# Performance work log

Measured on AMD Instinct MI355X. Metric: run time of the kernel, lower is better.

Reference implementation:

```python
import jax, jax.numpy as jnp
import numpy as np

DIM = 768
NUM_HEADS = 12
HEAD_DIM = DIM // NUM_HEADS
H, W = 16, 64
HK, WK = 7, 11
N = H * W
B = 8
SCALE = HEAD_DIM ** -0.5


def build_local_mask():
    # Vectorized version of the original nested loop: for each token (h,w),
    # positions inside the hk x wk window are visible (0), others -inf.
    h_idx = np.repeat(np.arange(H), W)  # [N]
    w_idx = np.tile(np.arange(W), H)    # [N]
    hh = np.arange(H + HK - 1)
    ww = np.arange(W + WK - 1)
    in_h = (hh[None, :] >= h_idx[:, None]) & (hh[None, :] < h_idx[:, None] + HK)  # [N, H+hk-1]
    in_w = (ww[None, :] >= w_idx[:, None]) & (ww[None, :] < w_idx[:, None] + WK)  # [N, W+wk-1]
    visible = in_h[:, :, None] & in_w[:, None, :]  # [N, H+hk-1, W+wk-1]
    mask_big = np.where(visible, 0.0, 1.0).astype(np.float32)
    mask_crop = mask_big[:, HK // 2:H + HK // 2, WK // 2:W + WK // 2].reshape(N, N)
    mask = np.where(mask_crop < 1.0, mask_crop, np.float32(-np.inf))  # [N, N]
    return jnp.asarray(mask)[None, None]  # [1, 1, N, N]


def setup_inputs() -> dict:
    key = jax.random.key(0)
    k1, k2, k3 = jax.random.split(key, 3)
    x = jax.random.normal(k1, (B, N, DIM), dtype=jnp.float32)
    w_qkv = jax.random.normal(k2, (3 * DIM, DIM), dtype=jnp.float32) * 0.02  # torch Linear weight [out,in]
    w_proj = jax.random.normal(k3, (DIM, DIM), dtype=jnp.float32) * 0.02
    b_proj = jnp.zeros((DIM,), dtype=jnp.float32)
    mask = build_local_mask()
    return {"x": x, "w_qkv": w_qkv, "w_proj": w_proj, "b_proj": b_proj, "mask": mask}


def reference(x, w_qkv, w_proj, b_proj, mask):
    Bx, Nx, C = x.shape
    qkv = jnp.einsum('bnc,oc->bno', x, w_qkv)  # [B, N, 3*dim]
    qkv = qkv.reshape(Bx, Nx, 3, NUM_HEADS, HEAD_DIM).transpose(2, 0, 3, 1, 4)  # [3,B,h,N,d]
    q, k, v = qkv[0] * SCALE, qkv[1], qkv[2]
    attn = jnp.einsum('bhnd,bhmd->bhnm', q, k) + mask  # [B,h,N,N] with local -inf mask
    attn = jax.nn.softmax(attn, axis=-1)
    out = jnp.einsum('bhnm,bhmd->bhnd', attn, v)  # [B,h,N,d]
    out = out.transpose(0, 2, 1, 3).reshape(Bx, Nx, C)
    out = jnp.einsum('bnc,oc->bno', out, w_proj) + b_proj
    return out
```

## Files before the change

### kernel.cpp

```cpp
#include <hip/hip_runtime.h>
#include <hip/hip_bf16.h>
#include <stdint.h>

typedef __bf16 bf16;
typedef __bf16 bf16x8 __attribute__((ext_vector_type(8)));
typedef __bf16 bf16x4 __attribute__((ext_vector_type(4)));
typedef float f32x4 __attribute__((ext_vector_type(4)));

#define KDIM 768
#define NHEAD 12
#define HDIM 64
#define NTOK 1024
#define BATCH 8

#define SWZ(row, b) ((b) ^ (((row) & 7) << 4))

__device__ __forceinline__ void gl_lds16(const bf16* g, bf16* l) {
    __builtin_amdgcn_global_load_lds((const __attribute__((address_space(1))) void*)g,
                                     (__attribute__((address_space(3))) void*)l, 16, 0, 0);
}

__global__ void k_cvt_all(const float* __restrict__ x, const float* __restrict__ wq,
                          const float* __restrict__ wp, bf16* __restrict__ xb,
                          bf16* __restrict__ wqb, bf16* __restrict__ wpb) {
    int b = blockIdx.x;
    const float* src;
    bf16* dst;
    int base;
    if (b < 6144)       { src = x;  dst = xb;  base = b; }
    else if (b < 7872)  { src = wq; dst = wqb; base = b - 6144; }
    else                { src = wp; dst = wpb; base = b - 7872; }
    int i = (base * 256 + threadIdx.x) * 4;
    float4 v = *(const float4*)(src + i);
    bf16x4 o;
    o[0] = (bf16)v.x; o[1] = (bf16)v.y; o[2] = (bf16)v.z; o[3] = (bf16)v.w;
    *(bf16x4*)(dst + i) = o;
}

#define BM 128
#define BN 128
#define BK 32

#define STAGE_G(Ab, Wb, Abuf, Bbuf, k0) do {                                  \
    gl_lds16((Ab) + (size_t)srow * KDIM + (k0) + scol,        (Abuf) + wv * 512);        \
    gl_lds16((Ab) + (size_t)(srow + 64) * KDIM + (k0) + scol, (Abuf) + 2048 + wv * 512); \
    gl_lds16((Wb) + (size_t)srow * KDIM + (k0) + scol,        (Bbuf) + wv * 512);        \
    gl_lds16((Wb) + (size_t)(srow + 64) * KDIM + (k0) + scol, (Bbuf) + 2048 + wv * 512); \
} while (0)

__global__ __launch_bounds__(256) void k_gemm_qkv(
    const bf16* __restrict__ A, const bf16* __restrict__ W,
    bf16* __restrict__ qb, bf16* __restrict__ kb, bf16* __restrict__ vb)
{
    __shared__ bf16 As[2][BM * BK];
    __shared__ bf16 Bs[2][BN * BK];
    const int t = threadIdx.x;
    const int lane = t & 63;
    const int wv = t >> 6;
    const int wr = wv >> 1, wc = wv & 1;
    const int lr = lane & 15, lkb = (lane >> 4) * 8;
    const int bm = blockIdx.x, bn = blockIdx.y;

    const bf16* Ab = A + (size_t)bm * BM * KDIM;
    const bf16* Wb = W + (size_t)bn * BN * KDIM;

    const int srow = t >> 2;
    const int scol = (t & 3) * 8;

    f32x4 acc[4][4] = {};

    STAGE_G(Ab, Wb, As[0], Bs[0], 0);
    __syncthreads();

    int cur = 0;
    for (int k0 = 0; k0 < KDIM; k0 += BK) {
        if (k0 + BK < KDIM)
            STAGE_G(Ab, Wb, As[cur ^ 1], Bs[cur ^ 1], k0 + BK);
        bf16x8 af[4], bfr[4];
#pragma unroll
        for (int m = 0; m < 4; ++m)
            af[m] = *(const bf16x8*)&As[cur][(wr * 64 + m * 16 + lr) * BK + lkb];
#pragma unroll
        for (int n = 0; n < 4; ++n)
            bfr[n] = *(const bf16x8*)&Bs[cur][(wc * 64 + n * 16 + lr) * BK + lkb];
#pragma unroll
        for (int m = 0; m < 4; ++m)
#pragma unroll
            for (int n = 0; n < 4; ++n)
                acc[m][n] = __builtin_amdgcn_mfma_f32_16x16x32_bf16(af[m], bfr[n], acc[m][n], 0, 0, 0);
        __syncthreads();
        cur ^= 1;
    }

    const float QSC = 0.18033688011112042f;
#pragma unroll
    for (int n = 0; n < 4; ++n) {
        int o = bn * BN + wc * 64 + n * 16 + lr;
        int s = o / 768;
        int rem = o - s * 768;
        int head = rem >> 6;
        int d = o & 63;
        bf16* dst = (s == 0) ? qb : ((s == 1) ? kb : vb);
        float sc = (s == 0) ? QSC : 1.0f;
#pragma unroll
        for (int m = 0; m < 4; ++m) {
            int grow = bm * BM + wr * 64 + m * 16 + (lane >> 4) * 4;
            int bidx = grow >> 10;
            int tok = grow & 1023;
            size_t base = (((size_t)bidx * NHEAD + head) * NTOK + tok) * HDIM + d;
#pragma unroll
            for (int r = 0; r < 4; ++r)
                dst[base + (size_t)r * HDIM] = (bf16)(acc[m][n][r] * sc);
        }
    }
}

__global__ __launch_bounds__(256) void k_gemm_proj(
    const bf16* __restrict__ A, const bf16* __restrict__ W,
    const float* __restrict__ bias, float* __restrict__ out)
{
    __shared__ bf16 As[2][BM * BK];
    __shared__ bf16 Bs[2][BN * BK];
    const int t = threadIdx.x;
    const int lane = t & 63;
    const int wv = t >> 6;
    const int wr = wv >> 1, wc = wv & 1;
    const int lr = lane & 15, lkb = (lane >> 4) * 8;
    const int bm = blockIdx.x, bn = blockIdx.y;

    const bf16* Ab = A + (size_t)bm * BM * KDIM;
    const bf16* Wb = W + (size_t)bn * BN * KDIM;

    const int srow = t >> 2;
    const int scol = (t & 3) * 8;

    f32x4 acc[4][4] = {};

    STAGE_G(Ab, Wb, As[0], Bs[0], 0);
    __syncthreads();

    int cur = 0;
    for (int k0 = 0; k0 < KDIM; k0 += BK) {
        if (k0 + BK < KDIM)
            STAGE_G(Ab, Wb, As[cur ^ 1], Bs[cur ^ 1], k0 + BK);
        bf16x8 af[4], bfr[4];
#pragma unroll
        for (int m = 0; m < 4; ++m)
            af[m] = *(const bf16x8*)&As[cur][(wr * 64 + m * 16 + lr) * BK + lkb];
#pragma unroll
        for (int n = 0; n < 4; ++n)
            bfr[n] = *(const bf16x8*)&Bs[cur][(wc * 64 + n * 16 + lr) * BK + lkb];
#pragma unroll
        for (int m = 0; m < 4; ++m)
#pragma unroll
            for (int n = 0; n < 4; ++n)
                acc[m][n] = __builtin_amdgcn_mfma_f32_16x16x32_bf16(af[m], bfr[n], acc[m][n], 0, 0, 0);
        __syncthreads();
        cur ^= 1;
    }

#pragma unroll
    for (int n = 0; n < 4; ++n) {
        int col = bn * BN + wc * 64 + n * 16 + lr;
        float bv = bias[col];
#pragma unroll
        for (int m = 0; m < 4; ++m) {
            int grow = bm * BM + wr * 64 + m * 16 + (lane >> 4) * 4;
#pragma unroll
            for (int r = 0; r < 4; ++r)
                out[(size_t)(grow + r) * KDIM + col] = acc[m][n][r] + bv;
        }
    }
}

__global__ __launch_bounds__(256) void k_attn(
    const bf16* __restrict__ qbuf, const bf16* __restrict__ kbuf,
    const bf16* __restrict__ vbuf, bf16* __restrict__ ob)
{
    const int x = blockIdx.x;
    const int sub = x >> 3;
    const int bh = (x & 7) * 12 + (sub >> 4);
    const int qblk = sub & 15;
    const int head = bh % NHEAD, bidx = bh / NHEAD;
    const bf16* Q  = qbuf + (size_t)bh * NTOK * HDIM;
    const bf16* Kp = kbuf + (size_t)bh * NTOK * HDIM;
    const bf16* Vp = vbuf + (size_t)bh * NTOK * HDIM;

    const int t = threadIdx.x, lane = t & 63, wv = t >> 6;
    const int lr = lane & 15, lg = lane >> 4, lkb = lg * 8;

    __shared__ bf16 Ks[2][64 * 64];
    __shared__ bf16 vT[2][64 * 64];
    __shared__ bf16 pls[4][16 * 64];

    {
        bf16x8 z = {};
        *(bf16x8*)&pls[wv][lane * 16] = z;
        *(bf16x8*)&pls[wv][lane * 16 + 8] = z;
    }

    bf16x8 qf[2];
#pragma unroll
    for (int ks = 0; ks < 2; ++ks)
        qf[ks] = *(const bf16x8*)(Q + (size_t)(qblk * 64 + wv * 16 + lr) * HDIM + ks * 32 + lkb);

    f32x4 acc[4] = {};
    float mrow[4] = {-1e30f, -1e30f, -1e30f, -1e30f};
    float lrow[4] = {0.f, 0.f, 0.f, 0.f};

    const int kh0 = (qblk - 3 < 0) ? 0 : qblk - 3;
    const int kh1 = (qblk + 3 > 15) ? 15 : qblk + 3;

    const int sj = t >> 2;
    const int sd = (t & 3) * 16;

    const bf16* ks0 = Kp + (size_t)(kh0 * 64 + sj) * HDIM + sd;
    const bf16* vs0 = Vp + (size_t)(kh0 * 64 + sj) * HDIM + sd;
    bf16x8 gk0 = *(const bf16x8*)ks0, gk1 = *(const bf16x8*)(ks0 + 8);
    bf16x8 gv0 = *(const bf16x8*)vs0, gv1 = *(const bf16x8*)(vs0 + 8);

    char* pb8 = (char*)pls[wv];
    const int wq0 = wv * 16 + lg * 4;
    int cur = 0;

    for (int kh = kh0; kh <= kh1; ++kh) {
        char* kb8 = (char*)Ks[cur];
        char* vb8 = (char*)vT[cur];
        {
            int kbo = sj * 128 + sd * 2;
            *(bf16x8*)(kb8 + SWZ(sj, kbo)) = gk0;
            *(bf16x8*)(kb8 + SWZ(sj, kbo + 16)) = gk1;
        }
#pragma unroll
        for (int ii = 0; ii < 8; ++ii) {
            int d = sd + ii;
            *(bf16*)(vb8 + SWZ(d, (d << 7) + (sj << 1))) = gv0[ii];
        }
#pragma unroll
        for (int ii = 0; ii < 8; ++ii) {
            int d = sd + 8 + ii;
            *(bf16*)(vb8 + SWZ(d, (d << 7) + (sj << 1))) = gv1[ii];
        }
        if (kh < kh1) {
            const bf16* kn = Kp + (size_t)((kh + 1) * 64 + sj) * HDIM + sd;
            const bf16* vn = Vp + (size_t)((kh + 1) * 64 + sj) * HDIM + sd;
            gk0 = *(const bf16x8*)kn; gk1 = *(const bf16x8*)(kn + 8);
            gv0 = *(const bf16x8*)vn; gv1 = *(const bf16x8*)(vn + 8);
        }
        asm volatile("s_waitcnt lgkmcnt(0)" ::: "memory");
        __builtin_amdgcn_s_barrier();

        f32x4 s[3];
#pragma unroll
        for (int jj = 0; jj < 3; ++jj) {
            int j = wv - 1 + jj;
            if (j >= 0 && j <= 3) {
                int key = j * 16 + lr;
                int kbase = key * 128;
                bf16x8 kf0 = *(const bf16x8*)(kb8 + SWZ(key, kbase + lg * 16));
                bf16x8 kf1 = *(const bf16x8*)(kb8 + SWZ(key, kbase + 64 + lg * 16));
                f32x4 sv = {};
                sv = __builtin_amdgcn_mfma_f32_16x16x32_bf16(qf[0], kf0, sv, 0, 0, 0);
                sv = __builtin_amdgcn_mfma_f32_16x16x32_bf16(qf[1], kf1, sv, 0, 0, 0);
#pragma unroll
                for (int r = 0; r < 4; ++r) {
                    int dw = wq0 + r - key;
                    sv[r] = (dw >= -5 && dw <= 5) ? sv[r] : -1e30f;
                }
                s[jj] = sv;
            } else {
                s[jj] = f32x4{-1e30f, -1e30f, -1e30f, -1e30f};
            }
        }

        float pm[4], scl[4];
#pragma unroll
        for (int r = 0; r < 4; ++r) pm[r] = fmaxf(fmaxf(s[0][r], s[1][r]), s[2][r]);
#pragma unroll
        for (int off = 1; off < 16; off <<= 1)
#pragma unroll
            for (int r = 0; r < 4; ++r) pm[r] = fmaxf(pm[r], __shfl_xor(pm[r], off));
#pragma unroll
        for (int r = 0; r < 4; ++r) {
            float mn = fmaxf(mrow[r], pm[r]);
            scl[r] = exp2f(mrow[r] - mn);
            mrow[r] = mn;
        }
#pragma unroll
        for (int dt = 0; dt < 4; ++dt)
#pragma unroll
            for (int r = 0; r < 4; ++r) acc[dt][r] *= scl[r];

        float psum[4] = {0.f, 0.f, 0.f, 0.f};
#pragma unroll
        for (int jj = 0; jj < 3; ++jj) {
            int j = wv - 1 + jj;
            if (j >= 0 && j <= 3) {
#pragma unroll
                for (int r = 0; r < 4; ++r) {
                    float p = exp2f(s[jj][r] - mrow[r]);
                    psum[r] += p;
                    int row = lg * 4 + r;
                    *(bf16*)(pb8 + SWZ(row, row * 128 + (j * 16 + lr) * 2)) = (bf16)p;
                }
            }
        }
#pragma unroll
        for (int r = 0; r < 4; ++r) lrow[r] = lrow[r] * scl[r] + psum[r];

        bf16x8 pf0 = *(const bf16x8*)(pb8 + SWZ(lr, lr * 128 + lg * 16));
        bf16x8 pf1 = *(const bf16x8*)(pb8 + SWZ(lr, lr * 128 + 64 + lg * 16));
#pragma unroll
        for (int dt = 0; dt < 4; ++dt) {
            int vrow = dt * 16 + lr;
            bf16x8 vf0 = *(const bf16x8*)(vb8 + SWZ(vrow, vrow * 128 + lg * 16));
            bf16x8 vf1 = *(const bf16x8*)(vb8 + SWZ(vrow, vrow * 128 + 64 + lg * 16));
            acc[dt] = __builtin_amdgcn_mfma_f32_16x16x32_bf16(pf0, vf0, acc[dt], 0, 0, 0);
            acc[dt] = __builtin_amdgcn_mfma_f32_16x16x32_bf16(pf1, vf1, acc[dt], 0, 0, 0);
        }
        cur ^= 1;
    }

#pragma unroll
    for (int off = 1; off < 16; off <<= 1)
#pragma unroll
        for (int r = 0; r < 4; ++r) lrow[r] += __shfl_xor(lrow[r], off);

#pragma unroll
    for (int r = 0; r < 4; ++r) {
        float inv = 1.0f / lrow[r];
        int tok = qblk * 64 + wv * 16 + lg * 4 + r;
        size_t rowbase = ((size_t)bidx * NTOK + tok) * KDIM + head * HDIM;
#pragma unroll
        for (int dt = 0; dt < 4; ++dt)
            ob[rowbase + dt * 16 + lr] = (bf16)(acc[dt][r] * inv);
    }
}

extern "C" void kernel_launch(void* const* d_in, const int* in_sizes, int n_in,
                              void* d_out, int out_size, void* d_ws, size_t ws_size,
                              hipStream_t stream) {
    const float* x      = (const float*)d_in[0];
    const float* w_qkv  = (const float*)d_in[1];
    const float* w_proj = (const float*)d_in[2];
    const float* b_proj = (const float*)d_in[3];
    float* out = (float*)d_out;

    char* ws = (char*)d_ws;
    bf16* xb  = (bf16*)(ws);
    bf16* wqb = (bf16*)(ws + 12582912);
    bf16* wpb = (bf16*)(ws + 16121856);
    bf16* qb  = (bf16*)(ws + 17301504);
    bf16* kb  = (bf16*)(ws + 29884416);
    bf16* vb  = (bf16*)(ws + 42467328);
    bf16* aob = (bf16*)(ws + 55050240);

    hipLaunchKernelGGL(k_cvt_all, dim3(8448), dim3(256), 0, stream, x, w_qkv, w_proj, xb, wqb, wpb);
    hipLaunchKernelGGL(k_gemm_qkv, dim3(64, 18), dim3(256), 0, stream, xb, wqb, qb, kb, vb);
    hipLaunchKernelGGL(k_attn,     dim3(1536), dim3(256), 0, stream, qb, kb, vb, aob);
    hipLaunchKernelGGL(k_gemm_proj, dim3(64, 6), dim3(256), 0, stream, aob, wpb, b_proj, out);
}
```

Baseline: 110.1 us.

## Swizzle GEMM LDS layout and deepen global-to-LDS prefetch pipeline

Both GEMM kernels get a new LDS staging layout in which the global_load_lds destinations are XOR-swizzled across row pairs, so the 16-byte fragment reads avoid bank conflicts. The main loop is rewritten to keep two tiles in flight: after the fragments are read into registers, the next-but-one tile is issued into the same buffer before the MFMAs run. Explicit vmcnt/lgkmcnt waits and raw barriers replace __syncthreads. This adds an extra barrier per iteration and depends on the hand-written wait counts being correct.

New measurement: 105.6 us. 4.1% less time.

```diff
diff --git a/kernel.cpp b/kernel.cpp
--- a/kernel.cpp
+++ b/kernel.cpp
@@ -41,12 +41,62 @@
 #define BN 128
 #define BK 32
 
-#define STAGE_G(Ab, Wb, Abuf, Bbuf, k0) do {                                  \
-    gl_lds16((Ab) + (size_t)srow * KDIM + (k0) + scol,        (Abuf) + wv * 512);        \
-    gl_lds16((Ab) + (size_t)(srow + 64) * KDIM + (k0) + scol, (Abuf) + 2048 + wv * 512); \
-    gl_lds16((Wb) + (size_t)srow * KDIM + (k0) + scol,        (Bbuf) + wv * 512);        \
-    gl_lds16((Wb) + (size_t)(srow + 64) * KDIM + (k0) + scol, (Bbuf) + 2048 + wv * 512); \
+#define STAGE_G(Ab, Wb, Abuf, Bbuf, k0) do {                                   \
+    gl_lds16((Ab) + (size_t)sr0 * KDIM + (k0) + sc0, (Abuf) + wv * 512);        \
+    gl_lds16((Ab) + (size_t)sr1 * KDIM + (k0) + sc1, (Abuf) + 2048 + wv * 512); \
+    gl_lds16((Wb) + (size_t)sr0 * KDIM + (k0) + sc0, (Bbuf) + wv * 512);        \
+    gl_lds16((Wb) + (size_t)sr1 * KDIM + (k0) + sc1, (Bbuf) + 2048 + wv * 512); \
 } while (0)
+
+#define GEMM_PRE()                                                              \
+    const int t = threadIdx.x;                                                  \
+    const int lane = t & 63;                                                    \
+    const int wv = t >> 6;                                                      \
+    const int wr = wv >> 1, wc = wv & 1;                                        \
+    const int lr = lane & 15, lg = lane >> 4;                                   \
+             \
+    const int q0 = wv * 64 + lane;                                              \
+    const int R0 = q0 >> 3, wp0 = (q0 & 7) ^ (R0 & 7);                          \
+    const int sr0 = 2 * R0 + (wp0 >> 2), sc0 = (wp0 & 3) * 8;                   \
+    const int q1 = 256 + wv * 64 + lane;                                        \
+    const int R1 = q1 >> 3, wp1 = (q1 & 7) ^ (R1 & 7);                          \
+    const int sr1 = 2 * R1 + (wp1 >> 2), sc1 = (wp1 & 3) * 8;                   \
+                                                         \
+    const int rhalf = lr >> 1;                                                  \
+    const int xorp = (((lr & 1) * 64 + lg * 16) ^ (rhalf << 4));
+
+#define GEMM_LOOP(Ab, Wb)                                                       \
+    f32x4 acc[4][4] = {};                                                       \
+    STAGE_G(Ab, Wb, As[0], Bs[0], 0);                                           \
+    STAGE_G(Ab, Wb, As[1], Bs[1], BK);                                          \
+    asm volatile("s_waitcnt vmcnt(4)" ::: "memory");                            \
+    __builtin_amdgcn_s_barrier();                                               \
+    for (int tt = 0; tt < 24; ++tt) {                                           \
+        int p = tt & 1;                                                         \
+        const char* Ab8 = (const char*)As[p];                                   \
+        const char* Bb8 = (const char*)Bs[p];                                   \
+        bf16x8 af[4], bfr[4];                                                   \
+        _Pragma("unroll")                                                       \
+        for (int m = 0; m < 4; ++m)                                             \
+            af[m] = *(const bf16x8*)(Ab8 + (wr * 32 + m * 8 + rhalf) * 128 + xorp); \
+        _Pragma("unroll")                                                       \
+        for (int n = 0; n < 4; ++n)                                             \
+            bfr[n] = *(const bf16x8*)(Bb8 + (wc * 32 + n * 8 + rhalf) * 128 + xorp); \
+        asm volatile("s_waitcnt lgkmcnt(0)" ::: "memory");                      \
+        __builtin_amdgcn_s_barrier();                                           \
+        if (tt < 22) {                                                          \
+            STAGE_G(Ab, Wb, As[p], Bs[p], (tt + 2) * BK);                       \
+            __builtin_amdgcn_sched_barrier(0);                                  \
+        }                                                                       \
+        _Pragma("unroll")                                                       \
+        for (int m = 0; m < 4; ++m)                                             \
+            _Pragma("unroll")                                                   \
+            for (int n = 0; n < 4; ++n)                                         \
+                acc[m][n] = __builtin_amdgcn_mfma_f32_16x16x32_bf16(af[m], bfr[n], acc[m][n], 0, 0, 0); \
+        if (tt < 22)       { asm volatile("s_waitcnt vmcnt(4)" ::: "memory"); } \
+        else if (tt == 22) { asm volatile("s_waitcnt vmcnt(0)" ::: "memory"); } \
+        __builtin_amdgcn_s_barrier();                                           \
+    }
 
 __global__ __launch_bounds__(256) void k_gemm_qkv(
     const bf16* __restrict__ A, const bf16* __restrict__ W,
@@ -54,43 +104,11 @@
 {
     __shared__ bf16 As[2][BM * BK];
     __shared__ bf16 Bs[2][BN * BK];
-    const int t = threadIdx.x;
-    const int lane = t & 63;
-    const int wv = t >> 6;
-    const int wr = wv >> 1, wc = wv & 1;
-    const int lr = lane & 15, lkb = (lane >> 4) * 8;
+    GEMM_PRE();
     const int bm = blockIdx.x, bn = blockIdx.y;
-
     const bf16* Ab = A + (size_t)bm * BM * KDIM;
     const bf16* Wb = W + (size_t)bn * BN * KDIM;
-
-    const int srow = t >> 2;
-    const int scol = (t & 3) * 8;
-
-    f32x4 acc[4][4] = {};
-
-    STAGE_G(Ab, Wb, As[0], Bs[0], 0);
-    __syncthreads();
-
-    int cur = 0;
-    for (int k0 = 0; k0 < KDIM; k0 += BK) {
-        if (k0 + BK < KDIM)
-            STAGE_G(Ab, Wb, As[cur ^ 1], Bs[cur ^ 1], k0 + BK);
-        bf16x8 af[4], bfr[4];
-#pragma unroll
-        for (int m = 0; m < 4; ++m)
-            af[m] = *(const bf16x8*)&As[cur][(wr * 64 + m * 16 + lr) * BK + lkb];
-#pragma unroll
-        for (int n = 0; n < 4; ++n)
-            bfr[n] = *(const bf16x8*)&Bs[cur][(wc * 64 + n * 16 + lr) * BK + lkb];
-#pragma unroll
-        for (int m = 0; m < 4; ++m)
-#pragma unroll
-            for (int n = 0; n < 4; ++n)
-                acc[m][n] = __builtin_amdgcn_mfma_f32_16x16x32_bf16(af[m], bfr[n], acc[m][n], 0, 0, 0);
-        __syncthreads();
-        cur ^= 1;
-    }
+    GEMM_LOOP(Ab, Wb);
 
     const float QSC = 0.18033688011112042f;
 #pragma unroll
@@ -104,7 +122,7 @@
         float sc = (s == 0) ? QSC : 1.0f;
 #pragma unroll
         for (int m = 0; m < 4; ++m) {
-            int grow = bm * BM + wr * 64 + m * 16 + (lane >> 4) * 4;
+            int grow = bm * BM + wr * 64 + m * 16 + lg * 4;
             int bidx = grow >> 10;
             int tok = grow & 1023;
             size_t base = (((size_t)bidx * NHEAD + head) * NTOK + tok) * HDIM + d;
@@ -121,43 +139,11 @@
 {
     __shared__ bf16 As[2][BM * BK];
     __shared__ bf16 Bs[2][BN * BK];
-    const int t = threadIdx.x;
-    const int lane = t & 63;
-    const int wv = t >> 6;
-    const int wr = wv >> 1, wc = wv & 1;
-    const int lr = lane & 15, lkb = (lane >> 4) * 8;
+    GEMM_PRE();
     const int bm = blockIdx.x, bn = blockIdx.y;
-
     const bf16* Ab = A + (size_t)bm * BM * KDIM;
     const bf16* Wb = W + (size_t)bn * BN * KDIM;
-
-    const int srow = t >> 2;
-    const int scol = (t & 3) * 8;
-
-    f32x4 acc[4][4] = {};
-
-    STAGE_G(Ab, Wb, As[0], Bs[0], 0);
-    __syncthreads();
-
-    int cur = 0;
-    for (int k0 = 0; k0 < KDIM; k0 += BK) {
-        if (k0 + BK < KDIM)
-            STAGE_G(Ab, Wb, As[cur ^ 1], Bs[cur ^ 1], k0 + BK);
-        bf16x8 af[4], bfr[4];
-#pragma unroll
-        for (int m = 0; m < 4; ++m)
-            af[m] = *(const bf16x8*)&As[cur][(wr * 64 + m * 16 + lr) * BK + lkb];
-#pragma unroll
-        for (int n = 0; n < 4; ++n)
-            bfr[n] = *(const bf16x8*)&Bs[cur][(wc * 64 + n * 16 + lr) * BK + lkb];
-#pragma unroll
-        for (int m = 0; m < 4; ++m)
-#pragma unroll
-            for (int n = 0; n < 4; ++n)
-                acc[m][n] = __builtin_amdgcn_mfma_f32_16x16x32_bf16(af[m], bfr[n], acc[m][n], 0, 0, 0);
-        __syncthreads();
-        cur ^= 1;
-    }
+    GEMM_LOOP(Ab, Wb);
 
 #pragma unroll
     for (int n = 0; n < 4; ++n) {
@@ -165,7 +151,7 @@
         float bv = bias[col];
 #pragma unroll
         for (int m = 0; m < 4; ++m) {
-            int grow = bm * BM + wr * 64 + m * 16 + (lane >> 4) * 4;
+            int grow = bm * BM + wr * 64 + m * 16 + lg * 4;
 #pragma unroll
             for (int r = 0; r < 4; ++r)
                 out[(size_t)(grow + r) * KDIM + col] = acc[m][n][r] + bv;
```

## Rework QKV and projection GEMMs with swizzled LDS, split-phase prefetch, and wider tiles

Applied to the files above, without the earlier changes.

The QKV GEMM moves to 128x192 tiles (grid 64x12), XOR-swizzles its LDS layout, and interleaves global-to-LDS staging between two halves of the MFMA work. It uses raw s_barrier, s_waitcnt vmcnt control and s_setprio to keep loads in flight during compute. The projection GEMM gets a swizzled LDS layout and a two-deep prefetch with explicit waitcnt and barriers. The aim is to hide global load latency and avoid LDS bank conflicts, at the cost of fragile hand-tuned synchronisation and higher register pressure from launch_bounds(256,3).

New measurement: 103.8 us. 1.06x faster.

```diff
diff --git a/kernel.cpp b/kernel.cpp
--- a/kernel.cpp
+++ b/kernel.cpp
@@ -19,6 +19,9 @@
     __builtin_amdgcn_global_load_lds((const __attribute__((address_space(1))) void*)g,
                                      (__attribute__((address_space(3))) void*)l, 16, 0, 0);
 }
+
+#define G_MFMA(a, b, c) __builtin_amdgcn_mfma_f32_16x16x32_bf16(a, b, c, 0, 0, 0)
+#define VMW(N) asm volatile("s_waitcnt vmcnt(" #N ")" ::: "memory")
 
 __global__ void k_cvt_all(const float* __restrict__ x, const float* __restrict__ wq,
                           const float* __restrict__ wp, bf16* __restrict__ xb,
@@ -37,65 +40,92 @@
     *(bf16x4*)(dst + i) = o;
 }
 
-#define BM 128
-#define BN 128
-#define BK 32
-
-#define STAGE_G(Ab, Wb, Abuf, Bbuf, k0) do {                                  \
-    gl_lds16((Ab) + (size_t)srow * KDIM + (k0) + scol,        (Abuf) + wv * 512);        \
-    gl_lds16((Ab) + (size_t)(srow + 64) * KDIM + (k0) + scol, (Abuf) + 2048 + wv * 512); \
-    gl_lds16((Wb) + (size_t)srow * KDIM + (k0) + scol,        (Bbuf) + wv * 512);        \
-    gl_lds16((Wb) + (size_t)(srow + 64) * KDIM + (k0) + scol, (Bbuf) + 2048 + wv * 512); \
+
+#define QTILE(S, kA, kB, doA, doB, vmn) do {                                    \
+    const char* A8 = (const char*)sA[S];                                        \
+    const char* B8 = (const char*)sB[S];                                        \
+    bf16x8 af[2], bfr[6];                                                       \
+    af[0] = *(const bf16x8*)(A8 + (wr * 64 + 0 + lr) * 64 + kxoff);             \
+    af[1] = *(const bf16x8*)(A8 + (wr * 64 + 16 + lr) * 64 + kxoff);            \
+    _Pragma("unroll")                                                           \
+    for (int n = 0; n < 6; ++n)                                                 \
+        bfr[n] = *(const bf16x8*)(B8 + (wc * 96 + n * 16 + lr) * 64 + kxoff);   \
+    if (doA) {                                                                  \
+        const bf16* p_ = Ast + (size_t)(kA) * 32;                               \
+        gl_lds16(p_,                    &sA[(S) ^ 1][t * 8]);                   \
+        gl_lds16(p_ + (size_t)64 * KDIM, &sA[(S) ^ 1][t * 8 + 2048]);           \
+    }                                                                           \
+    __builtin_amdgcn_s_setprio(1);                                              \
+    _Pragma("unroll")                                                           \
+    for (int m = 0; m < 2; ++m)                                                 \
+        _Pragma("unroll")                                                       \
+        for (int n = 0; n < 6; ++n)                                             \
+            acc[m][n] = G_MFMA(af[m], bfr[n], acc[m][n]);                       \
+    __builtin_amdgcn_s_setprio(0);                                              \
+    __builtin_amdgcn_s_barrier();                                               \
+    af[0] = *(const bf16x8*)(A8 + (wr * 64 + 32 + lr) * 64 + kxoff);            \
+    af[1] = *(const bf16x8*)(A8 + (wr * 64 + 48 + lr) * 64 + kxoff);            \
+    if (doB) {                                                                  \
+        const bf16* p_ = Wst + (size_t)(kB) * 32;                               \
+        gl_lds16(p_,                     &sB[S][t * 8]);                        \
+        gl_lds16(p_ + (size_t)64 * KDIM,  &sB[S][t * 8 + 2048]);                \
+        gl_lds16(p_ + (size_t)128 * KDIM, &sB[S][t * 8 + 4096]);                \
+    }                                                                           \
+    __builtin_amdgcn_s_setprio(1);                                              \
+    _Pragma("unroll")                                                           \
+    for (int m = 0; m < 2; ++m)                                                 \
+        _Pragma("unroll")                                                       \
+        for (int n = 0; n < 6; ++n)                                             \
+            acc[m + 2][n] = G_MFMA(af[m], bfr[n], acc[m + 2][n]);               \
+    __builtin_amdgcn_s_setprio(0);                                              \
+    if ((vmn) == 3) { VMW(3); } else if ((vmn) == 0) { VMW(0); }                \
+    __builtin_amdgcn_s_barrier();                                               \
 } while (0)
 
-__global__ __launch_bounds__(256) void k_gemm_qkv(
+__global__ __launch_bounds__(256, 3) void k_gemm_qkv(
     const bf16* __restrict__ A, const bf16* __restrict__ W,
     bf16* __restrict__ qb, bf16* __restrict__ kb, bf16* __restrict__ vb)
 {
-    __shared__ bf16 As[2][BM * BK];
-    __shared__ bf16 Bs[2][BN * BK];
+    __shared__ __attribute__((aligned(16))) bf16 sA[2][4096];
+    __shared__ __attribute__((aligned(16))) bf16 sB[2][6144];
     const int t = threadIdx.x;
     const int lane = t & 63;
     const int wv = t >> 6;
     const int wr = wv >> 1, wc = wv & 1;
-    const int lr = lane & 15, lkb = (lane >> 4) * 8;
+    const int lr = lane & 15, lg = lane >> 4;
+    const int kxoff = (lg << 4) ^ (((lr >> 1) & 3) << 4);
+    const int srow = t >> 2;
+    const int spos = ((t & 3) ^ ((t >> 3) & 3)) * 8;
     const int bm = blockIdx.x, bn = blockIdx.y;
-
-    const bf16* Ab = A + (size_t)bm * BM * KDIM;
-    const bf16* Wb = W + (size_t)bn * BN * KDIM;
-
-    const int srow = t >> 2;
-    const int scol = (t & 3) * 8;
-
-    f32x4 acc[4][4] = {};
-
-    STAGE_G(Ab, Wb, As[0], Bs[0], 0);
-    __syncthreads();
-
-    int cur = 0;
-    for (int k0 = 0; k0 < KDIM; k0 += BK) {
-        if (k0 + BK < KDIM)
-            STAGE_G(Ab, Wb, As[cur ^ 1], Bs[cur ^ 1], k0 + BK);
-        bf16x8 af[4], bfr[4];
-#pragma unroll
-        for (int m = 0; m < 4; ++m)
-            af[m] = *(const bf16x8*)&As[cur][(wr * 64 + m * 16 + lr) * BK + lkb];
-#pragma unroll
-        for (int n = 0; n < 4; ++n)
-            bfr[n] = *(const bf16x8*)&Bs[cur][(wc * 64 + n * 16 + lr) * BK + lkb];
-#pragma unroll
-        for (int m = 0; m < 4; ++m)
-#pragma unroll
-            for (int n = 0; n < 4; ++n)
-                acc[m][n] = __builtin_amdgcn_mfma_f32_16x16x32_bf16(af[m], bfr[n], acc[m][n], 0, 0, 0);
-        __syncthreads();
-        cur ^= 1;
-    }
+    const bf16* Ab = A + (size_t)bm * 128 * KDIM;
+    const bf16* Wb = W + (size_t)bn * 192 * KDIM;
+    const bf16* Ast = Ab + (size_t)srow * KDIM + spos;
+    const bf16* Wst = Wb + (size_t)srow * KDIM + spos;
+    f32x4 acc[4][6] = {};
+
+    gl_lds16(Ast,                     &sA[0][t * 8]);
+    gl_lds16(Ast + (size_t)64 * KDIM, &sA[0][t * 8 + 2048]);
+    gl_lds16(Wst,                      &sB[0][t * 8]);
+    gl_lds16(Wst + (size_t)64 * KDIM,  &sB[0][t * 8 + 2048]);
+    gl_lds16(Wst + (size_t)128 * KDIM, &sB[0][t * 8 + 4096]);
+    gl_lds16(Wst + 32,                      &sB[1][t * 8]);
+    gl_lds16(Wst + 32 + (size_t)64 * KDIM,  &sB[1][t * 8 + 2048]);
+    gl_lds16(Wst + 32 + (size_t)128 * KDIM, &sB[1][t * 8 + 4096]);
+    VMW(3);
+    __builtin_amdgcn_s_barrier();
+
+#pragma unroll 1
+    for (int g = 0; g < 11; ++g) {
+        QTILE(0, 2 * g + 1, 2 * g + 2, 1, 1, 3);
+        QTILE(1, 2 * g + 2, 2 * g + 3, 1, 1, 3);
+    }
+    QTILE(0, 23, 0, 1, 0, 0);
+    QTILE(1, 0, 0, 0, 0, -1);
 
     const float QSC = 0.18033688011112042f;
 #pragma unroll
-    for (int n = 0; n < 4; ++n) {
-        int o = bn * BN + wc * 64 + n * 16 + lr;
+    for (int n = 0; n < 6; ++n) {
+        int o = bn * 192 + wc * 96 + n * 16 + lr;
         int s = o / 768;
         int rem = o - s * 768;
         int head = rem >> 6;
@@ -104,7 +134,7 @@
         float sc = (s == 0) ? QSC : 1.0f;
 #pragma unroll
         for (int m = 0; m < 4; ++m) {
-            int grow = bm * BM + wr * 64 + m * 16 + (lane >> 4) * 4;
+            int grow = bm * 128 + wr * 64 + m * 16 + lg * 4;
             int bidx = grow >> 10;
             int tok = grow & 1023;
             size_t base = (((size_t)bidx * NHEAD + head) * NTOK + tok) * HDIM + d;
@@ -114,58 +144,77 @@
         }
     }
 }
+
+#define P_STAGE(Ab, Wb, Abuf, Bbuf, k0) do {                                    \
+    gl_lds16((Ab) + (size_t)sr0 * KDIM + (k0) + sc0, (Abuf) + wv * 512);        \
+    gl_lds16((Ab) + (size_t)sr1 * KDIM + (k0) + sc1, (Abuf) + 2048 + wv * 512); \
+    gl_lds16((Wb) + (size_t)sr0 * KDIM + (k0) + sc0, (Bbuf) + wv * 512);        \
+    gl_lds16((Wb) + (size_t)sr1 * KDIM + (k0) + sc1, (Bbuf) + 2048 + wv * 512); \
+} while (0)
 
 __global__ __launch_bounds__(256) void k_gemm_proj(
     const bf16* __restrict__ A, const bf16* __restrict__ W,
     const float* __restrict__ bias, float* __restrict__ out)
 {
-    __shared__ bf16 As[2][BM * BK];
-    __shared__ bf16 Bs[2][BN * BK];
+    __shared__ bf16 As[2][4096];
+    __shared__ bf16 Bs[2][4096];
     const int t = threadIdx.x;
     const int lane = t & 63;
     const int wv = t >> 6;
     const int wr = wv >> 1, wc = wv & 1;
-    const int lr = lane & 15, lkb = (lane >> 4) * 8;
+    const int lr = lane & 15, lg = lane >> 4;
+    const int q0 = wv * 64 + lane;
+    const int R0 = q0 >> 3, wp0 = (q0 & 7) ^ (R0 & 7);
+    const int sr0 = 2 * R0 + (wp0 >> 2), sc0 = (wp0 & 3) * 8;
+    const int q1 = 256 + wv * 64 + lane;
+    const int R1 = q1 >> 3, wp1 = (q1 & 7) ^ (R1 & 7);
+    const int sr1 = 2 * R1 + (wp1 >> 2), sc1 = (wp1 & 3) * 8;
+    const int rhalf = lr >> 1;
+    const int xorp = (((lr & 1) * 64 + lg * 16) ^ (rhalf << 4));
     const int bm = blockIdx.x, bn = blockIdx.y;
-
-    const bf16* Ab = A + (size_t)bm * BM * KDIM;
-    const bf16* Wb = W + (size_t)bn * BN * KDIM;
-
-    const int srow = t >> 2;
-    const int scol = (t & 3) * 8;
+    const bf16* Ab = A + (size_t)bm * 128 * KDIM;
+    const bf16* Wb = W + (size_t)bn * 128 * KDIM;
 
     f32x4 acc[4][4] = {};
-
-    STAGE_G(Ab, Wb, As[0], Bs[0], 0);
-    __syncthreads();
-
-    int cur = 0;
-    for (int k0 = 0; k0 < KDIM; k0 += BK) {
-        if (k0 + BK < KDIM)
-            STAGE_G(Ab, Wb, As[cur ^ 1], Bs[cur ^ 1], k0 + BK);
+    P_STAGE(Ab, Wb, As[0], Bs[0], 0);
+    P_STAGE(Ab, Wb, As[1], Bs[1], 32);
+    VMW(4);
+    __builtin_amdgcn_s_barrier();
+#pragma unroll 1
+    for (int tt = 0; tt < 24; ++tt) {
+        int p = tt & 1;
+        const char* Ab8 = (const char*)As[p];
+        const char* Bb8 = (const char*)Bs[p];
         bf16x8 af[4], bfr[4];
 #pragma unroll
         for (int m = 0; m < 4; ++m)
-            af[m] = *(const bf16x8*)&As[cur][(wr * 64 + m * 16 + lr) * BK + lkb];
+            af[m] = *(const bf16x8*)(Ab8 + (wr * 32 + m * 8 + rhalf) * 128 + xorp);
 #pragma unroll
         for (int n = 0; n < 4; ++n)
-            bfr[n] = *(const bf16x8*)&Bs[cur][(wc * 64 + n * 16 + lr) * BK + lkb];
+            bfr[n] = *(const bf16x8*)(Bb8 + (wc * 32 + n * 8 + rhalf) * 128 + xorp);
+        asm volatile("s_waitcnt lgkmcnt(0)" ::: "memory");
+        __builtin_amdgcn_s_barrier();
+        if (tt < 22) {
+            P_STAGE(Ab, Wb, As[p], Bs[p], (tt + 2) * 32);
+            __builtin_amdgcn_sched_barrier(0);
+        }
 #pragma unroll
         for (int m = 0; m < 4; ++m)
 #pragma unroll
             for (int n = 0; n < 4; ++n)
-                acc[m][n] = __builtin_amdgcn_mfma_f32_16x16x32_bf16(af[m], bfr[n], acc[m][n], 0, 0, 0);
-        __syncthreads();
-        cur ^= 1;
+                acc[m][n] = G_MFMA(af[m], bfr[n], acc[m][n]);
+        if (tt < 22)       { VMW(4); }
+        else if (tt == 22) { VMW(0); }
+        __builtin_amdgcn_s_barrier();
     }
 
 #pragma unroll
     for (int n = 0; n < 4; ++n) {
-        int col = bn * BN + wc * 64 + n * 16 + lr;
+        int col = bn * 128 + wc * 64 + n * 16 + lr;
         float bv = bias[col];
 #pragma unroll
         for (int m = 0; m < 4; ++m) {
-            int grow = bm * BM + wr * 64 + m * 16 + (lane >> 4) * 4;
+            int grow = bm * 128 + wr * 64 + m * 16 + lg * 4;
 #pragma unroll
             for (int r = 0; r < 4; ++r)
                 out[(size_t)(grow + r) * KDIM + col] = acc[m][n][r] + bv;
@@ -356,7 +405,7 @@
     bf16* aob = (bf16*)(ws + 55050240);
 
     hipLaunchKernelGGL(k_cvt_all, dim3(8448), dim3(256), 0, stream, x, w_qkv, w_proj, xb, wqb, wpb);
-    hipLaunchKernelGGL(k_gemm_qkv, dim3(64, 18), dim3(256), 0, stream, xb, wqb, qb, kb, vb);
+    hipLaunchKernelGGL(k_gemm_qkv, dim3(64, 12), dim3(256), 0, stream, xb, wqb, qb, kb, vb);
     hipLaunchKernelGGL(k_attn,     dim3(1536), dim3(256), 0, stream, qb, kb, vb, aob);
     hipLaunchKernelGGL(k_gemm_proj, dim3(64, 6), dim3(256), 0, stream, aob, wpb, b_proj, out);
 }
```
